# Optimization experiments

Measured on AMD Instinct MI355X. Metric: run time of the kernel, lower is better.

The kernel has to match this reference:

```python
import jax, jax.numpy as jnp
import numpy as np

ALPHA = 1.0
TOL = 1e-5
MAX_ITER = 50
M = 0.05  # monotonicity margin of MONSingleFc


def setup_inputs() -> dict:
    key = jax.random.key(0)
    kx, ku, kub, ka, kb = jax.random.split(key, 5)
    batch, in_dim, d = 65536, 128, 128
    x = jax.random.normal(kx, (batch, in_dim), jnp.float32)
    Uw = jax.random.normal(ku, (d, in_dim), jnp.float32) / np.sqrt(in_dim)
    ub = jax.random.normal(kub, (d,), jnp.float32) * 0.1
    A = jax.random.normal(ka, (d, d), jnp.float32) / np.sqrt(d)
    B = jax.random.normal(kb, (d, d), jnp.float32) / np.sqrt(d)
    return {"x": x, "Uw": Uw, "ub": ub, "A": A, "B": B}


def _multiply(z, A, B):
    # W z with W = (1-m) I - A^T A + B - B^T ; torch Linear applies z @ W^T
    return (1.0 - M) * z - (z @ A.T) @ A + z @ B.T - z @ B


def _solve_pr(bias, Winv):
    # Peaceman-Rachford fixed point: z = relu(W z + bias)
    def cond(s):
        _, _, err, it = s
        return (err > TOL) & (it < MAX_ITER)

    def body(s):
        z, u, _, it = s
        u12 = 2.0 * z - u
        z12 = (u12 + ALPHA * bias) @ Winv.T  # linear inverse solve
        u_new = 2.0 * z12 - u12
        zn = jax.nn.relu(u_new)
        err = jnp.linalg.norm(zn - z) / (1e-6 + jnp.linalg.norm(zn))
        return zn, u_new, err, it + 1

    z0 = jnp.zeros_like(bias)
    z, _, _, _ = jax.lax.while_loop(
        cond, body, (z0, z0, jnp.asarray(1.0, bias.dtype), 0)
    )
    return z


def reference(x, Uw, ub, A, B):
    d = A.shape[0]
    I = jnp.eye(d, dtype=A.dtype)
    W = (1.0 - M) * I - A.T @ A + B - B.T
    # init_inverse(1 + alpha, -alpha)
    Winv = jnp.linalg.inv((1.0 + ALPHA) * I - ALPHA * W)
    bias = x @ Uw.T + ub  # U(x)
    z_star = _solve_pr(bias, Winv)  # no-grad fixed point
    # final application: nonlin(linear(x, z*))
    return jax.nn.relu(bias + _multiply(z_star, A, B))
```

## Files before the change

### kernel.cpp

```cpp
#include <hip/hip_runtime.h>

#define D 128

typedef __attribute__((ext_vector_type(2))) float f32x2;
typedef __attribute__((ext_vector_type(4))) float f32x4;
typedef __attribute__((ext_vector_type(16))) float f32x16;
typedef __attribute__((ext_vector_type(8))) _Float16 f16x8;
typedef __attribute__((ext_vector_type(2))) __fp16 fp16v2;
typedef __attribute__((ext_vector_type(4))) unsigned int u32x4;

__device__ __forceinline__ void split2(float a, float b, unsigned &hi, unsigned &lo) {
  fp16v2 h = __builtin_amdgcn_cvt_pkrtz(a, b);
  float ra = a - (float)h[0];
  float rb = b - (float)h[1];
  fp16v2 lv = __builtin_amdgcn_cvt_pkrtz(ra, rb);
  hi = __builtin_bit_cast(unsigned, h);
  lo = __builtin_bit_cast(unsigned, lv);
}

__device__ __forceinline__ f32x16 mm(u32x4 a, u32x4 b, f32x16 c) {
  return __builtin_amdgcn_mfma_f32_32x32x16_f16(
      __builtin_bit_cast(f16x8, a), __builtin_bit_cast(f16x8, b), c, 0, 0, 0);
}

__device__ __forceinline__ f32x16 zero16() {
  f32x16 z;
#pragma unroll
  for (int e = 0; e < 16; ++e) z[e] = 0.f;
  return z;
}

__global__ void wmat_kernel(const float* __restrict__ A, const float* __restrict__ B,
                            float* __restrict__ W, float* __restrict__ Mm) {
  const int i = blockIdx.x;
  const int j = threadIdx.x;
  float s = 0.f;
#pragma unroll 8
  for (int k = 0; k < D; ++k) s = fmaf(A[k * D + i], A[k * D + j], s);
  const float diag = (i == j) ? 1.f : 0.f;
  const float w = 0.95f * diag - s + B[i * D + j] - B[j * D + i];
  W[i * D + j] = w;
  Mm[i * D + j] = 2.f * diag - w;
}

__global__ __launch_bounds__(1024) void inv_kernel(const float* __restrict__ Mm,
                                                   float* __restrict__ Winv) {
  __shared__ float rowbuf[2][2 * D];
  __shared__ __align__(16) float colbuf[2][D];
  const int t = threadIdx.x;
  const int c = t & 255;
  const int rb = t >> 8;
  const int r0 = rb * 32;
  float aug[32];
#pragma unroll
  for (int rr = 0; rr < 32; ++rr) {
    const int r = r0 + rr;
    aug[rr] = (c < D) ? Mm[r * D + c] : ((c - D == r) ? 1.f : 0.f);
  }
  if (rb == 0) rowbuf[0][c] = aug[0];
  if (c == 0) {
#pragma unroll
    for (int rr = 0; rr < 32; ++rr) colbuf[0][r0 + rr] = aug[rr];
  }
  __syncthreads();
  for (int k = 0; k < D; ++k) {
    const int p = k & 1;
    const float invp = 1.f / rowbuf[p][k];
    const float pr = rowbuf[p][c] * invp;
    float cb[32];
#pragma unroll
    for (int q = 0; q < 8; ++q) {
      f32x4 v = *(const f32x4*)&colbuf[p][r0 + 4 * q];
      cb[4 * q] = v[0]; cb[4 * q + 1] = v[1];
      cb[4 * q + 2] = v[2]; cb[4 * q + 3] = v[3];
    }
#pragma unroll
    for (int rr = 0; rr < 32; ++rr) {
      const int r = r0 + rr;
      aug[rr] = (r == k) ? pr : fmaf(-cb[rr], pr, aug[rr]);
    }
    if (k + 1 < D) {
      float rv = 0.f;
#pragma unroll
      for (int rr = 0; rr < 32; ++rr)
        if (rr == ((k + 1) & 31)) rv = aug[rr];
      if (rb == ((k + 1) >> 5)) rowbuf[p ^ 1][c] = rv;
      if (c == k + 1) {
#pragma unroll
        for (int rr = 0; rr < 32; ++rr) colbuf[p ^ 1][r0 + rr] = aug[rr];
      }
    }
    __syncthreads();
  }
  if (c >= D) {
#pragma unroll
    for (int rr = 0; rr < 32; ++rr) Winv[(r0 + rr) * D + (c - D)] = aug[rr];
  }
}

__global__ __launch_bounds__(256, 1) void mon_main(
    const float* __restrict__ x, const float* __restrict__ Uw,
    const float* __restrict__ ub, const float* __restrict__ Wg,
    const float* __restrict__ Winvg, float* __restrict__ out) {

  __shared__ u32x4 AH[2048];
  __shared__ u32x4 AL[2048];
  __shared__ float UB[D];

  const int tid = threadIdx.x;
  const int w = tid >> 6;
  const int l = tid & 63;
  const int l5 = l & 31;
  const int hi5 = l >> 5;
  const int rg = blockIdx.x * 128 + w * 32 + l5;

  const int base_g = l5 * 16 + (hi5 ^ (l5 & 7));
  const int vub = hi5 * 16;
  const float* xr = x + (size_t)rg * D + hi5 * 8;

  f32x16 acc[4];
  float t[4][16];
  float bw[4][16];

  auto stageAB = [&](const float* __restrict__ M, float s) {
#pragma unroll
    for (int it = 0; it < 8; ++it) {
      const int G = tid + it * 256;
      const int i = G >> 4, g = G & 15;
      const float* src = M + i * D + g * 8;
      f32x4 a = *(const f32x4*)src;
      f32x4 b = *(const f32x4*)(src + 4);
      unsigned h0, l0_, h1, l1_, h2_, l2_, h3, l3_;
      split2(s * a[0], s * a[1], h0, l0_);
      split2(s * a[2], s * a[3], h1, l1_);
      split2(s * b[0], s * b[1], h2_, l2_);
      split2(s * b[2], s * b[3], h3, l3_);
      const int pg = g ^ (i & 7);
      AH[i * 16 + pg] = (u32x4){h0, h1, h2_, h3};
      AL[i * 16 + pg] = (u32x4){l0_, l1_, l2_, l3_};
    }
  };

  auto mfma_pass = [&](bool useAbs) {
#pragma unroll
    for (int kt = 0; kt < 8; ++kt) {
      const int jt = kt >> 1;
      const int eb = 8 * (kt & 1);
      unsigned oh[4], ol[4];
#pragma unroll
      for (int q = 0; q < 4; ++q) {
        float a0 = t[jt][eb + 2 * q], a1 = t[jt][eb + 2 * q + 1];
        if (useAbs) { a0 = __builtin_fabsf(a0); a1 = __builtin_fabsf(a1); }
        split2(a0, a1, oh[q], ol[q]);
      }
      u32x4 fH, fL;
#pragma unroll
      for (int b = 0; b < 2; ++b) {
        auto rh = __builtin_amdgcn_permlane32_swap(oh[b], oh[2 + b], false, false);
        auto rl = __builtin_amdgcn_permlane32_swap(ol[b], ol[2 + b], false, false);
        fH[b] = rh[0]; fH[2 + b] = rh[1];
        fL[b] = rl[0]; fL[2 + b] = rl[1];
      }
      const int gx = base_g ^ (2 * kt);
#pragma unroll
      for (int ft = 0; ft < 4; ++ft) {
        const u32x4 ah = AH[ft * 512 + gx];
        const u32x4 al = AL[ft * 512 + gx];
        acc[ft] = mm(ah, fH, kt == 0 ? zero16() : acc[ft]);
        acc[ft] = mm(ah, fL, acc[ft]);
        acc[ft] = mm(al, fH, acc[ft]);
      }
    }
  };

  auto x_pass = [&]() {
#pragma unroll
    for (int kt = 0; kt < 8; ++kt) {
      f32x4 xa = *(const f32x4*)(xr + kt * 16);
      f32x4 xb = *(const f32x4*)(xr + kt * 16 + 4);
      unsigned h0, l0_, h1, l1_, h2_, l2_, h3, l3_;
      split2(xa[0], xa[1], h0, l0_);
      split2(xa[2], xa[3], h1, l1_);
      split2(xb[0], xb[1], h2_, l2_);
      split2(xb[2], xb[3], h3, l3_);
      u32x4 fh = (u32x4){h0, h1, h2_, h3};
      u32x4 fl = (u32x4){l0_, l1_, l2_, l3_};
      const int gx = base_g ^ (2 * kt);
#pragma unroll
      for (int ft = 0; ft < 4; ++ft) {
        const u32x4 ah = AH[ft * 512 + gx];
        const u32x4 al = AL[ft * 512 + gx];
        acc[ft] = mm(ah, fh, kt == 0 ? zero16() : acc[ft]);
        acc[ft] = mm(ah, fl, acc[ft]);
        acc[ft] = mm(al, fh, acc[ft]);
      }
    }
  };

  stageAB(Uw, 1.f);
  if (tid < D) UB[tid] = ub[tid];
  __syncthreads();
  x_pass();
#pragma unroll
  for (int ft = 0; ft < 4; ++ft)
#pragma unroll
    for (int e2 = 0; e2 < 8; ++e2) {
      const int i0 = 32 * ft + 2 * (e2 & 1) + 8 * (e2 >> 1);
      f32x2 ubp = *(const f32x2*)((const char*)UB + vub + 4 * i0);
      t[ft][2 * e2] = acc[ft][2 * e2] + ubp[0];
      t[ft][2 * e2 + 1] = acc[ft][2 * e2 + 1] + ubp[1];
    }
  __syncthreads();
  stageAB(Winvg, 2.f);
  __syncthreads();

  mfma_pass(false);
#pragma unroll
  for (int ft = 0; ft < 4; ++ft)
#pragma unroll
    for (int e = 0; e < 16; ++e) {
      const float b = 0.5f * acc[ft][e];
      bw[ft][e] = b;
      t[ft][e] = b;
    }

#pragma unroll 1
  for (int it = 0; it < 48; ++it) {
    mfma_pass(true);
#pragma unroll
    for (int ft = 0; ft < 4; ++ft)
#pragma unroll
      for (int e = 0; e < 16; ++e)
        t[ft][e] = (acc[ft][e] + bw[ft][e]) - __builtin_fabsf(t[ft][e]);
  }

  mfma_pass(true);
#pragma unroll
  for (int ft = 0; ft < 4; ++ft)
#pragma unroll
    for (int e = 0; e < 16; ++e)
      t[ft][e] = fmaxf((acc[ft][e] + bw[ft][e]) - __builtin_fabsf(t[ft][e]), 0.f);

  __syncthreads();
  stageAB(Wg, 2.f);
  __syncthreads();
  mfma_pass(false);
#pragma unroll
  for (int ft = 0; ft < 4; ++ft)
#pragma unroll
    for (int e = 0; e < 16; ++e) bw[ft][e] = acc[ft][e];

  __syncthreads();
  stageAB(Uw, 1.f);
  __syncthreads();
  x_pass();
  float* op = out + (size_t)rg * D;
#pragma unroll
  for (int ft = 0; ft < 4; ++ft)
#pragma unroll
    for (int e2 = 0; e2 < 8; ++e2) {
      const int i0 = 32 * ft + 2 * (e2 & 1) + 8 * (e2 >> 1);
      f32x2 ubp = *(const f32x2*)((const char*)UB + vub + 4 * i0);
      float o0 = fmaxf(acc[ft][2 * e2] + ubp[0] + bw[ft][2 * e2], 0.f);
      float o1 = fmaxf(acc[ft][2 * e2 + 1] + ubp[1] + bw[ft][2 * e2 + 1], 0.f);
      *(f32x2*)(op + i0 + 4 * hi5) = (f32x2){o0, o1};
    }
}

extern "C" void kernel_launch(void* const* d_in, const int* in_sizes, int n_in,
                              void* d_out, int out_size, void* d_ws, size_t ws_size,
                              hipStream_t stream) {
  const float* x = (const float*)d_in[0];
  const float* Uw = (const float*)d_in[1];
  const float* ub = (const float*)d_in[2];
  const float* A = (const float*)d_in[3];
  const float* B = (const float*)d_in[4];
  float* out = (float*)d_out;

  float* W = (float*)d_ws;
  float* Mm = W + D * D;
  float* Winv = W + 2 * D * D;

  wmat_kernel<<<D, D, 0, stream>>>(A, B, W, Mm);
  inv_kernel<<<1, 1024, 0, stream>>>(Mm, Winv);

  const int batch = in_sizes[0] / D;
  mon_main<<<batch / 128, 256, 0, stream>>>(x, Uw, ub, W, Winv, out);
}
```

Baseline: 471.4 us.

## Block Gauss-Jordan inverse by 4 pivots and fold bias into MFMA accumulator init

The matrix inversion kernel now eliminates four pivot rows per step, with a small 4x4 block inverse. This cuts the number of block-wide barriers from 128 to 32. In the main kernel the per-iteration bias add is removed by seeding the MFMA accumulator with the bias vector. The Winv/W scaling is adjusted so the factor 0.5 is no longer needed, and ub is read directly from global memory instead of shared memory. Risks are slightly different rounding from the block pivoting and extra accumulator registers.

Result: faster. 417.2 us (-11.5%).

```diff
diff --git a/kernel.cpp b/kernel.cpp
--- a/kernel.cpp
+++ b/kernel.cpp
@@ -45,8 +45,8 @@
 
 __global__ __launch_bounds__(1024) void inv_kernel(const float* __restrict__ Mm,
                                                    float* __restrict__ Winv) {
-  __shared__ float rowbuf[2][2 * D];
-  __shared__ __align__(16) float colbuf[2][D];
+  __shared__ float PROW[2][4][256];
+  __shared__ __align__(16) float PC[2][D][4];
   const int t = threadIdx.x;
   const int c = t & 255;
   const int rb = t >> 8;
@@ -57,37 +57,72 @@
     const int r = r0 + rr;
     aug[rr] = (c < D) ? Mm[r * D + c] : ((c - D == r) ? 1.f : 0.f);
   }
-  if (rb == 0) rowbuf[0][c] = aug[0];
-  if (c == 0) {
-#pragma unroll
-    for (int rr = 0; rr < 32; ++rr) colbuf[0][r0 + rr] = aug[rr];
-  }
-  __syncthreads();
-  for (int k = 0; k < D; ++k) {
-    const int p = k & 1;
-    const float invp = 1.f / rowbuf[p][k];
-    const float pr = rowbuf[p][c] * invp;
-    float cb[32];
-#pragma unroll
-    for (int q = 0; q < 8; ++q) {
-      f32x4 v = *(const f32x4*)&colbuf[p][r0 + 4 * q];
-      cb[4 * q] = v[0]; cb[4 * q + 1] = v[1];
-      cb[4 * q + 2] = v[2]; cb[4 * q + 3] = v[3];
-    }
+  if (rb == 0) {
+#pragma unroll
+    for (int s = 0; s < 4; ++s) PROW[0][s][c] = aug[s];
+  }
+  if (c < 4) {
+#pragma unroll
+    for (int rr = 0; rr < 32; ++rr) PC[0][r0 + rr][c] = aug[rr];
+  }
+  __syncthreads();
+#pragma unroll
+  for (int p = 0; p < 32; ++p) {
+    const int buf = p & 1;
+    const int kp = 4 * p;
+    float p4[4], Bk[4][4], Bi[4][4];
+#pragma unroll
+    for (int s = 0; s < 4; ++s) p4[s] = PROW[buf][s][c];
+#pragma unroll
+    for (int s = 0; s < 4; ++s)
+#pragma unroll
+      for (int j = 0; j < 4; ++j) {
+        Bk[s][j] = PROW[buf][s][kp + j];
+        Bi[s][j] = (s == j) ? 1.f : 0.f;
+      }
+#pragma unroll
+    for (int k = 0; k < 4; ++k) {
+      const float ip = 1.f / Bk[k][k];
+#pragma unroll
+      for (int j = 0; j < 4; ++j) { Bk[k][j] *= ip; Bi[k][j] *= ip; }
+#pragma unroll
+      for (int s = 0; s < 4; ++s)
+        if (s != k) {
+          const float f = Bk[s][k];
+#pragma unroll
+          for (int j = 0; j < 4; ++j) {
+            Bk[s][j] = fmaf(-f, Bk[k][j], Bk[s][j]);
+            Bi[s][j] = fmaf(-f, Bi[k][j], Bi[s][j]);
+          }
+        }
+    }
+    float y[4];
+#pragma unroll
+    for (int s = 0; s < 4; ++s)
+      y[s] = fmaf(Bi[s][0], p4[0], fmaf(Bi[s][1], p4[1],
+             fmaf(Bi[s][2], p4[2], Bi[s][3] * p4[3])));
 #pragma unroll
     for (int rr = 0; rr < 32; ++rr) {
-      const int r = r0 + rr;
-      aug[rr] = (r == k) ? pr : fmaf(-cb[rr], pr, aug[rr]);
-    }
-    if (k + 1 < D) {
-      float rv = 0.f;
-#pragma unroll
-      for (int rr = 0; rr < 32; ++rr)
-        if (rr == ((k + 1) & 31)) rv = aug[rr];
-      if (rb == ((k + 1) >> 5)) rowbuf[p ^ 1][c] = rv;
-      if (c == k + 1) {
-#pragma unroll
-        for (int rr = 0; rr < 32; ++rr) colbuf[p ^ 1][r0 + rr] = aug[rr];
+      f32x4 c4 = *(const f32x4*)&PC[buf][r0 + rr][0];
+      aug[rr] = fmaf(-c4[0], y[0], fmaf(-c4[1], y[1],
+                fmaf(-c4[2], y[2], fmaf(-c4[3], y[3], aug[rr]))));
+    }
+    if (rb == (kp >> 5)) {
+      const int base = kp & 31;
+#pragma unroll
+      for (int s = 0; s < 4; ++s) aug[base + s] = y[s];
+    }
+    if (p + 1 < 32) {
+      const int kn = kp + 4;
+      const int nb = buf ^ 1;
+      if (rb == (kn >> 5)) {
+        const int nbase = kn & 31;
+#pragma unroll
+        for (int s = 0; s < 4; ++s) PROW[nb][s][c] = aug[nbase + s];
+      }
+      if (c >= kn && c < kn + 4) {
+#pragma unroll
+        for (int rr = 0; rr < 32; ++rr) PC[nb][r0 + rr][c - kn] = aug[rr];
       }
     }
     __syncthreads();
@@ -105,7 +140,6 @@
 
   __shared__ u32x4 AH[2048];
   __shared__ u32x4 AL[2048];
-  __shared__ float UB[D];
 
   const int tid = threadIdx.x;
   const int w = tid >> 6;
@@ -115,12 +149,11 @@
   const int rg = blockIdx.x * 128 + w * 32 + l5;
 
   const int base_g = l5 * 16 + (hi5 ^ (l5 & 7));
-  const int vub = hi5 * 16;
   const float* xr = x + (size_t)rg * D + hi5 * 8;
 
   f32x16 acc[4];
+  f32x16 bwC[4];
   float t[4][16];
-  float bw[4][16];
 
   auto stageAB = [&](const float* __restrict__ M, float s) {
 #pragma unroll
@@ -141,7 +174,7 @@
     }
   };
 
-  auto mfma_pass = [&](bool useAbs) {
+  auto mfma_pass = [&](bool useAbs, bool useC) {
 #pragma unroll
     for (int kt = 0; kt < 8; ++kt) {
       const int jt = kt >> 1;
@@ -166,14 +199,14 @@
       for (int ft = 0; ft < 4; ++ft) {
         const u32x4 ah = AH[ft * 512 + gx];
         const u32x4 al = AL[ft * 512 + gx];
-        acc[ft] = mm(ah, fH, kt == 0 ? zero16() : acc[ft]);
+        acc[ft] = mm(ah, fH, kt == 0 ? (useC ? bwC[ft] : zero16()) : acc[ft]);
         acc[ft] = mm(ah, fL, acc[ft]);
         acc[ft] = mm(al, fH, acc[ft]);
       }
     }
   };
 
-  auto x_pass = [&]() {
+  auto x_pass = [&](bool useC) {
 #pragma unroll
     for (int kt = 0; kt < 8; ++kt) {
       f32x4 xa = *(const f32x4*)(xr + kt * 16);
@@ -190,7 +223,7 @@
       for (int ft = 0; ft < 4; ++ft) {
         const u32x4 ah = AH[ft * 512 + gx];
         const u32x4 al = AL[ft * 512 + gx];
-        acc[ft] = mm(ah, fh, kt == 0 ? zero16() : acc[ft]);
+        acc[ft] = mm(ah, fh, kt == 0 ? (useC ? bwC[ft] : zero16()) : acc[ft]);
         acc[ft] = mm(ah, fl, acc[ft]);
         acc[ft] = mm(al, fh, acc[ft]);
       }
@@ -198,15 +231,14 @@
   };
 
   stageAB(Uw, 1.f);
-  if (tid < D) UB[tid] = ub[tid];
-  __syncthreads();
-  x_pass();
+  __syncthreads();
+  x_pass(false);
 #pragma unroll
   for (int ft = 0; ft < 4; ++ft)
 #pragma unroll
     for (int e2 = 0; e2 < 8; ++e2) {
       const int i0 = 32 * ft + 2 * (e2 & 1) + 8 * (e2 >> 1);
-      f32x2 ubp = *(const f32x2*)((const char*)UB + vub + 4 * i0);
+      f32x2 ubp = *(const f32x2*)(ub + i0 + 4 * hi5);
       t[ft][2 * e2] = acc[ft][2 * e2] + ubp[0];
       t[ft][2 * e2 + 1] = acc[ft][2 * e2 + 1] + ubp[1];
     }
@@ -214,55 +246,51 @@
   stageAB(Winvg, 2.f);
   __syncthreads();
 
-  mfma_pass(false);
-#pragma unroll
-  for (int ft = 0; ft < 4; ++ft)
-#pragma unroll
-    for (int e = 0; e < 16; ++e) {
-      const float b = 0.5f * acc[ft][e];
-      bw[ft][e] = b;
-      t[ft][e] = b;
-    }
+  mfma_pass(false, false);
+#pragma unroll
+  for (int ft = 0; ft < 4; ++ft) {
+    bwC[ft] = acc[ft];
+#pragma unroll
+    for (int e = 0; e < 16; ++e) t[ft][e] = acc[ft][e];
+  }
 
 #pragma unroll 1
   for (int it = 0; it < 48; ++it) {
-    mfma_pass(true);
+    mfma_pass(true, true);
 #pragma unroll
     for (int ft = 0; ft < 4; ++ft)
 #pragma unroll
       for (int e = 0; e < 16; ++e)
-        t[ft][e] = (acc[ft][e] + bw[ft][e]) - __builtin_fabsf(t[ft][e]);
-  }
-
-  mfma_pass(true);
+        t[ft][e] = acc[ft][e] - __builtin_fabsf(t[ft][e]);
+  }
+
+  mfma_pass(true, true);
 #pragma unroll
   for (int ft = 0; ft < 4; ++ft)
 #pragma unroll
     for (int e = 0; e < 16; ++e)
-      t[ft][e] = fmaxf((acc[ft][e] + bw[ft][e]) - __builtin_fabsf(t[ft][e]), 0.f);
-
-  __syncthreads();
-  stageAB(Wg, 2.f);
-  __syncthreads();
-  mfma_pass(false);
-#pragma unroll
-  for (int ft = 0; ft < 4; ++ft)
-#pragma unroll
-    for (int e = 0; e < 16; ++e) bw[ft][e] = acc[ft][e];
+      t[ft][e] = fmaxf(acc[ft][e] - __builtin_fabsf(t[ft][e]), 0.f);
+
+  __syncthreads();
+  stageAB(Wg, 1.f);
+  __syncthreads();
+  mfma_pass(false, false);
+#pragma unroll
+  for (int ft = 0; ft < 4; ++ft) bwC[ft] = acc[ft];
 
   __syncthreads();
   stageAB(Uw, 1.f);
   __syncthreads();
-  x_pass();
+  x_pass(true);
   float* op = out + (size_t)rg * D;
 #pragma unroll
   for (int ft = 0; ft < 4; ++ft)
 #pragma unroll
     for (int e2 = 0; e2 < 8; ++e2) {
       const int i0 = 32 * ft + 2 * (e2 & 1) + 8 * (e2 >> 1);
-      f32x2 ubp = *(const f32x2*)((const char*)UB + vub + 4 * i0);
-      float o0 = fmaxf(acc[ft][2 * e2] + ubp[0] + bw[ft][2 * e2], 0.f);
-      float o1 = fmaxf(acc[ft][2 * e2 + 1] + ubp[1] + bw[ft][2 * e2 + 1], 0.f);
+      f32x2 ubp = *(const f32x2*)(ub + i0 + 4 * hi5);
+      float o0 = fmaxf(acc[ft][2 * e2] + ubp[0], 0.f);
+      float o1 = fmaxf(acc[ft][2 * e2 + 1] + ubp[1], 0.f);
       *(f32x2*)(op + i0 + 4 * hi5) = (f32x2){o0, o1};
     }
 }
```
